# Kernel tuning notes

Measured on AMD Instinct MI355X. Metric: run time of the kernel, lower is better.

Reference implementation:

```python
import jax, jax.numpy as jnp
import numpy as np

B, IN, H = 4096, 1024, 1024

def setup_inputs() -> dict:
    key = jax.random.key(0)
    ks = jax.random.split(key, 8)
    s = 1.0 / np.sqrt(IN + H)  # ~torch Linear init scale
    return {
        "x": jax.random.normal(ks[0], (B, IN), jnp.float32),
        "h_prev": jax.random.normal(ks[1], (B, H), jnp.float32),
        "c_prev": jax.random.normal(ks[2], (B, H), jnp.float32),
        "Wf": jax.random.normal(ks[3], (IN + H, H), jnp.float32) * s,
        "bf": jnp.zeros((H,), jnp.float32),
        "Wi": jax.random.normal(ks[4], (IN + H, H), jnp.float32) * s,
        "bi": jnp.zeros((H,), jnp.float32),
        "Wg": jax.random.normal(ks[5], (IN + H, H), jnp.float32) * s,
        "bg": jnp.zeros((H,), jnp.float32),
        "Wo": jax.random.normal(ks[6], (IN + H, H), jnp.float32) * s,
        "bo": jnp.zeros((H,), jnp.float32),
    }

def reference(x, h_prev, c_prev, Wf, bf, Wi, bi, Wg, bg, Wo, bo):
    combined = jnp.concatenate([x, h_prev], axis=1)          # [B, IN+H]
    # fuse the 4 gate projections into one GEMM: [B, IN+H] x [IN+H, 4H]
    W = jnp.concatenate([Wf, Wi, Wg, Wo], axis=1)            # [IN+H, 4H]
    b = jnp.concatenate([bf, bi, bg, bo], axis=0)            # [4H]
    gates = combined @ W + b                                  # [B, 4H]
    f_t, i_t, g_t, o_t = jnp.split(gates, 4, axis=1)
    f_t = jax.nn.sigmoid(f_t)
    i_t = jax.nn.sigmoid(i_t)
    g_t = jnp.tanh(g_t)
    o_t = jax.nn.sigmoid(o_t)
    c_next = f_t * c_prev + i_t * g_t
    h_next = o_t * jnp.tanh(c_next)
    return (h_next, c_next)
```

## Files before the change

kernel.cpp:

```cpp
#include <hip/hip_runtime.h>

#define B_DIM 4096
#define H_DIM 1024
#define K_DIM 2048

typedef unsigned short u16;
typedef unsigned int u32;
typedef __attribute__((ext_vector_type(8))) short short8;
typedef __attribute__((ext_vector_type(4))) float f32x4;

typedef const __attribute__((address_space(1))) void* gas_ptr;
typedef __attribute__((address_space(3))) void* las_ptr;

#define WT_ELEMS (4 * H_DIM * K_DIM)
#define AC_ELEMS (B_DIM * K_DIM)
#define WS_NEEDED ((size_t)(WT_ELEMS + AC_ELEMS) * 2)

__device__ __forceinline__ void gl_lds16(const u16* g, u16* l) {
    __builtin_amdgcn_global_load_lds((gas_ptr)g, (las_ptr)l, 16, 0, 0);
}
__device__ __forceinline__ float bf2f(u16 v) {
    return __builtin_bit_cast(float, (u32)((u32)v << 16));
}
__device__ __forceinline__ u16 f2bf(float f) {
    u32 u = __builtin_bit_cast(u32, f);
    return (u16)((u + 0x7fffu + ((u >> 16) & 1u)) >> 16);
}
__device__ __forceinline__ float sigm(float x) { return 1.0f / (1.0f + __expf(-x)); }
__device__ __forceinline__ float tanh_f(float x) { return 1.0f - 2.0f / (__expf(2.0f * x) + 1.0f); }

__global__ __launch_bounds__(256) void prep_all(const float* __restrict__ x, const float* __restrict__ h,
                                                const float* __restrict__ Wf, const float* __restrict__ Wi,
                                                const float* __restrict__ Wg, const float* __restrict__ Wo,
                                                u16* __restrict__ A, u16* __restrict__ Wt) {
    __shared__ u16 tl[64][72];
    const int t = threadIdx.x;
    if (blockIdx.x < 4096) {
        int e = (blockIdx.x * 256 + t) * 8;
        int m = e >> 11, c = e & 2047;
        const float* src = (c < 1024) ? (x + (size_t)m * 1024 + c) : (h + (size_t)m * 1024 + (c - 1024));
        float4 v0 = ((const float4*)src)[0], v1 = ((const float4*)src)[1];
        short8 q;
        q[0] = (short)f2bf(v0.x); q[1] = (short)f2bf(v0.y); q[2] = (short)f2bf(v0.z); q[3] = (short)f2bf(v0.w);
        q[4] = (short)f2bf(v1.x); q[5] = (short)f2bf(v1.y); q[6] = (short)f2bf(v1.z); q[7] = (short)f2bf(v1.w);
        *(short8*)(A + e) = q;
    } else {
        int bid = blockIdx.x - 4096;
        const int k0 = (bid & 31) * 64, n0 = ((bid >> 5) & 15) * 64, g = bid >> 9;
        const float* W = (g == 0) ? Wf : (g == 1) ? Wi : (g == 2) ? Wg : Wo;
        {
            int kl = t >> 2, nc = (t & 3) * 16;
            const float4* src = (const float4*)(W + (size_t)(k0 + kl) * H_DIM + n0 + nc);
            float4 v0 = src[0], v1 = src[1], v2 = src[2], v3 = src[3];
            short8 q0, q1;
            q0[0] = (short)f2bf(v0.x); q0[1] = (short)f2bf(v0.y); q0[2] = (short)f2bf(v0.z); q0[3] = (short)f2bf(v0.w);
            q0[4] = (short)f2bf(v1.x); q0[5] = (short)f2bf(v1.y); q0[6] = (short)f2bf(v1.z); q0[7] = (short)f2bf(v1.w);
            q1[0] = (short)f2bf(v2.x); q1[1] = (short)f2bf(v2.y); q1[2] = (short)f2bf(v2.z); q1[3] = (short)f2bf(v2.w);
            q1[4] = (short)f2bf(v3.x); q1[5] = (short)f2bf(v3.y); q1[6] = (short)f2bf(v3.z); q1[7] = (short)f2bf(v3.w);
            *(short8*)&tl[kl][nc] = q0;
            *(short8*)&tl[kl][nc + 8] = q1;
        }
        __syncthreads();
        {
            int nl = t >> 2, kc = (t & 3) * 16;
            short8 r0, r1;
#pragma unroll
            for (int j = 0; j < 8; ++j) { r0[j] = (short)tl[kc + j][nl]; r1[j] = (short)tl[kc + 8 + j][nl]; }
            u16* dst = Wt + (size_t)g * (H_DIM * K_DIM) + (size_t)(n0 + nl) * K_DIM + k0 + kc;
            *(short8*)dst = r0;
            *(short8*)(dst + 8) = r1;
        }
    }
}

__global__ __launch_bounds__(256) void lstm_gemm(
    const u16* __restrict__ A, const u16* __restrict__ Wt, const float* __restrict__ c_prev,
    const float* __restrict__ bf_, const float* __restrict__ bi_,
    const float* __restrict__ bg_, const float* __restrict__ bo_,
    float* __restrict__ out) {
    __shared__ u16 sA[128 * 64];
    __shared__ u16 sB[4 * 32 * 64];

    const int t = threadIdx.x;
    const int w = t >> 6;
    const int l = t & 63;
    const int quad = l >> 4;
    const int l15 = l & 15;
    const int wr = w >> 1;
    const int wc = w & 1;
    const int m0 = blockIdx.x * 128;
    const int j0 = blockIdx.y * 32;

    f32x4 acc[4][4];
#pragma unroll
    for (int g = 0; g < 4; ++g)
#pragma unroll
        for (int mi = 0; mi < 4; ++mi)
            acc[g][mi] = (f32x4){0.f, 0.f, 0.f, 0.f};

    const u16* pA[4];
    const u16* pB[4];
#pragma unroll
    for (int i = 0; i < 4; ++i) {
        int c = i * 256 + t;
        int m = c >> 3, slot = c & 7;
        pA[i] = A + (size_t)(m0 + m) * K_DIM + (slot ^ (m & 7)) * 8;
    }
#pragma unroll
    for (int i = 0; i < 4; ++i) {
        int c = i * 256 + t;
        int g = c >> 8, r = c & 255;
        int n = r >> 3, slot = r & 7;
        pB[i] = Wt + (size_t)g * (H_DIM * K_DIM) + (size_t)(j0 + n) * K_DIM + (slot ^ (n & 7)) * 8;
    }
    const int v7 = l15 & 7;

    for (int kt = 0; kt < K_DIM / 64; ++kt) {
        __syncthreads();
#pragma unroll
        for (int i = 0; i < 4; ++i) {
            gl_lds16(pA[i], sA + (i * 256 + t) * 8);
            pA[i] += 64;
        }
#pragma unroll
        for (int i = 0; i < 4; ++i) {
            gl_lds16(pB[i], sB + (i * 256 + t) * 8);
            pB[i] += 64;
        }
        __syncthreads();

#pragma unroll
        for (int s = 0; s < 2; ++s) {
            const int sl = ((s * 4 + quad) ^ v7) * 8;
            short8 bfr[4];
#pragma unroll
            for (int g = 0; g < 4; ++g)
                bfr[g] = *(const short8*)(sB + g * 2048 + (wc * 16 + l15) * 64 + sl);
            short8 afr[4];
#pragma unroll
            for (int mi = 0; mi < 4; ++mi)
                afr[mi] = *(const short8*)(sA + (wr * 64 + mi * 16 + l15) * 64 + sl);
#pragma unroll
            for (int g = 0; g < 4; ++g)
#pragma unroll
                for (int mi = 0; mi < 4; ++mi)
                    acc[g][mi] = __builtin_amdgcn_mfma_f32_16x16x32_bf16(afr[mi], bfr[g], acc[g][mi], 0, 0, 0);
        }
    }

    const int col = j0 + wc * 16 + l15;
    const float bF = bf_[col], bI = bi_[col], bG = bg_[col], bO = bo_[col];
#pragma unroll
    for (int mi = 0; mi < 4; ++mi) {
        const int rowbase = m0 + wr * 64 + mi * 16 + quad * 4;
        float cp[4];
#pragma unroll
        for (int rr = 0; rr < 4; ++rr)
            cp[rr] = c_prev[(size_t)(rowbase + rr) * H_DIM + col];
#pragma unroll
        for (int rr = 0; rr < 4; ++rr) {
            float fv = sigm(acc[0][mi][rr] + bF);
            float iv = sigm(acc[1][mi][rr] + bI);
            float gv = tanh_f(acc[2][mi][rr] + bG);
            float ov = sigm(acc[3][mi][rr] + bO);
            float cn = fv * cp[rr] + iv * gv;
            float hn = ov * tanh_f(cn);
            size_t idx = (size_t)(rowbase + rr) * H_DIM + col;
            out[idx] = hn;
            out[(size_t)B_DIM * H_DIM + idx] = cn;
        }
    }
}

__global__ __launch_bounds__(256) void lstm_f32(
    const float* __restrict__ x, const float* __restrict__ h_prev, const float* __restrict__ c_prev,
    const float* __restrict__ Wf, const float* __restrict__ Wi, const float* __restrict__ Wg, const float* __restrict__ Wo,
    const float* __restrict__ bf_, const float* __restrict__ bi_, const float* __restrict__ bg_, const float* __restrict__ bo_,
    float* __restrict__ out) {
    __shared__ u16 smem[16384];
    u16* sA = smem;
    u16* sB = smem + 4096;

    const int t = threadIdx.x;
    const int w = t >> 6;
    const int l = t & 63;
    const int quad = l >> 4;
    const int l15 = l & 15;
    const int wr = w >> 1;
    const int wc = w & 1;
    const int m0 = blockIdx.x * 128;
    const int j0 = blockIdx.y * 32;

    const int arow = t >> 1;
    const int akh = (t & 1) * 16;
    const int r7 = t & 127;
    const int bk = r7 >> 2;
    const int bn8 = (r7 & 3) * 8;
    const int kswz = ((((bk >> 3) ^ (bn8 >> 3)) << 3) | (bk & 7));
    const float* WpA = (t < 128) ? Wf : Wi;
    const float* WpB = (t < 128) ? Wg : Wo;
    const int gA = (t >> 7);
    const int gB = 2 + (t >> 7);

    f32x4 acc[2][4][2];
#pragma unroll
    for (int gi = 0; gi < 2; ++gi)
#pragma unroll
        for (int mi = 0; mi < 4; ++mi)
#pragma unroll
            for (int ni = 0; ni < 2; ++ni)
                acc[gi][mi][ni] = (f32x4){0.f, 0.f, 0.f, 0.f};

    for (int kt = 0; kt < K_DIM / 32; ++kt) {
        const float* srcA = (kt < 32) ? x : h_prev;
        const int koff = (kt & 31) * 32;
        __syncthreads();

        const float4* ap = (const float4*)(srcA + (size_t)(m0 + arow) * H_DIM + koff + akh);
        float4 a0 = ap[0], a1 = ap[1], a2 = ap[2], a3 = ap[3];
        short8 p0, p1;
        p0[0] = (short)f2bf(a0.x); p0[1] = (short)f2bf(a0.y); p0[2] = (short)f2bf(a0.z); p0[3] = (short)f2bf(a0.w);
        p0[4] = (short)f2bf(a1.x); p0[5] = (short)f2bf(a1.y); p0[6] = (short)f2bf(a1.z); p0[7] = (short)f2bf(a1.w);
        p1[0] = (short)f2bf(a2.x); p1[1] = (short)f2bf(a2.y); p1[2] = (short)f2bf(a2.z); p1[3] = (short)f2bf(a2.w);
        p1[4] = (short)f2bf(a3.x); p1[5] = (short)f2bf(a3.y); p1[6] = (short)f2bf(a3.z); p1[7] = (short)f2bf(a3.w);
        *(short8*)(sA + arow * 32 + akh) = p0;
        *(short8*)(sA + arow * 32 + akh + 8) = p1;

        const float* gpA = WpA + (size_t)(kt * 32 + bk) * H_DIM + j0 + bn8;
        const float* gpB = WpB + (size_t)(kt * 32 + bk) * H_DIM + j0 + bn8;
        float4 c0 = *(const float4*)gpA, c1 = *(const float4*)(gpA + 4);
        float4 d0 = *(const float4*)gpB, d1 = *(const float4*)(gpB + 4);
        sB[gA * 1024 + (bn8 + 0) * 32 + kswz] = f2bf(c0.x);
        sB[gA * 1024 + (bn8 + 1) * 32 + kswz] = f2bf(c0.y);
        sB[gA * 1024 + (bn8 + 2) * 32 + kswz] = f2bf(c0.z);
        sB[gA * 1024 + (bn8 + 3) * 32 + kswz] = f2bf(c0.w);
        sB[gA * 1024 + (bn8 + 4) * 32 + kswz] = f2bf(c1.x);
        sB[gA * 1024 + (bn8 + 5) * 32 + kswz] = f2bf(c1.y);
        sB[gA * 1024 + (bn8 + 6) * 32 + kswz] = f2bf(c1.z);
        sB[gA * 1024 + (bn8 + 7) * 32 + kswz] = f2bf(c1.w);
        sB[gB * 1024 + (bn8 + 0) * 32 + kswz] = f2bf(d0.x);
        sB[gB * 1024 + (bn8 + 1) * 32 + kswz] = f2bf(d0.y);
        sB[gB * 1024 + (bn8 + 2) * 32 + kswz] = f2bf(d0.z);
        sB[gB * 1024 + (bn8 + 3) * 32 + kswz] = f2bf(d0.w);
        sB[gB * 1024 + (bn8 + 4) * 32 + kswz] = f2bf(d1.x);
        sB[gB * 1024 + (bn8 + 5) * 32 + kswz] = f2bf(d1.y);
        sB[gB * 1024 + (bn8 + 6) * 32 + kswz] = f2bf(d1.z);
        sB[gB * 1024 + (bn8 + 7) * 32 + kswz] = f2bf(d1.w);
        __syncthreads();

        short8 bfr[2][2];
#pragma unroll
        for (int gi = 0; gi < 2; ++gi) {
            int g = wc * 2 + gi;
#pragma unroll
            for (int ni = 0; ni < 2; ++ni) {
                int n = ni * 16 + l15;
                bfr[gi][ni] = *(const short8*)(sB + g * 1024 + n * 32 + ((quad ^ (n >> 3)) * 8));
            }
        }
#pragma unroll
        for (int mi = 0; mi < 4; ++mi) {
            int m = wr * 64 + mi * 16 + l15;
            short8 afr = *(const short8*)(sA + m * 32 + quad * 8);
#pragma unroll
            for (int gi = 0; gi < 2; ++gi)
#pragma unroll
                for (int ni = 0; ni < 2; ++ni)
                    acc[gi][mi][ni] =
                        __builtin_amdgcn_mfma_f32_16x16x32_bf16(afr, bfr[gi][ni], acc[gi][mi][ni], 0, 0, 0);
        }
    }

    __syncthreads();
#pragma unroll
    for (int gi = 0; gi < 2; ++gi) {
        int g = wc * 2 + gi;
        const float* bp = (g == 0) ? bf_ : (g == 1) ? bi_ : (g == 2) ? bg_ : bo_;
#pragma unroll
        for (int ni = 0; ni < 2; ++ni) {
            int col = ni * 16 + l15;
            float bias = bp[j0 + col];
#pragma unroll
            for (int mi = 0; mi < 4; ++mi)
#pragma unroll
                for (int rr = 0; rr < 4; ++rr) {
                    int row = wr * 64 + mi * 16 + quad * 4 + rr;
                    float v = acc[gi][mi][ni][rr] + bias;
                    v = (g == 2) ? tanh_f(v) : sigm(v);
                    smem[g * 4096 + row * 32 + col] = f2bf(v);
                }
        }
    }
    __syncthreads();

    const int col = t & 31;
    const int rb = t >> 5;
#pragma unroll
    for (int p = 0; p < 16; ++p) {
        int row = p * 8 + rb;
        float fv = bf2f(smem[0 * 4096 + row * 32 + col]);
        float iv = bf2f(smem[1 * 4096 + row * 32 + col]);
        float gv = bf2f(smem[2 * 4096 + row * 32 + col]);
        float ov = bf2f(smem[3 * 4096 + row * 32 + col]);
        size_t oidx = (size_t)(m0 + row) * H_DIM + j0 + col;
        float cp = c_prev[oidx];
        float cn = fv * cp + iv * gv;
        float hn = ov * tanh_f(cn);
        out[oidx] = hn;
        out[(size_t)B_DIM * H_DIM + oidx] = cn;
    }
}

extern "C" void kernel_launch(void* const* d_in, const int* in_sizes, int n_in,
                              void* d_out, int out_size, void* d_ws, size_t ws_size,
                              hipStream_t stream) {
    const float* x   = (const float*)d_in[0];
    const float* hp  = (const float*)d_in[1];
    const float* cp  = (const float*)d_in[2];
    const float* Wf  = (const float*)d_in[3];
    const float* bf_ = (const float*)d_in[4];
    const float* Wi  = (const float*)d_in[5];
    const float* bi_ = (const float*)d_in[6];
    const float* Wg  = (const float*)d_in[7];
    const float* bg_ = (const float*)d_in[8];
    const float* Wo  = (const float*)d_in[9];
    const float* bo_ = (const float*)d_in[10];

    if (ws_size >= WS_NEEDED) {
        u16* Wt = (u16*)d_ws;
        u16* Ac = (u16*)d_ws + WT_ELEMS;
        prep_all<<<dim3(4096 + 2048), dim3(256), 0, stream>>>(x, hp, Wf, Wi, Wg, Wo, Ac, Wt);
        lstm_gemm<<<dim3(B_DIM / 128, H_DIM / 32), dim3(256), 0, stream>>>(
            Ac, Wt, cp, bf_, bi_, bg_, bo_, (float*)d_out);
    } else {
        lstm_f32<<<dim3(B_DIM / 128, H_DIM / 32), dim3(256), 0, stream>>>(
            x, hp, cp, Wf, Wi, Wg, Wo, bf_, bi_, bg_, bo_, (float*)d_out);
    }
}
```

Before: 211.9 us.

## Enlarge GEMM block tile to 256 rows with per-warp 64x128 subtiles

Doubles the M tile per block from 128 to 256 rows and changes the warp layout so each warp computes 64 rows across all 32 columns of all four gates (8 N-subtiles), doubling accumulators per thread. This raises arithmetic intensity per LDS load and halves redundant weight tile loads from global memory. It costs more registers and LDS per block, which reduces occupancy; the grid shrinks to 512 blocks, and launch bounds now request 2 blocks per SM.

```diff
diff --git a/kernel.cpp b/kernel.cpp
--- a/kernel.cpp
+++ b/kernel.cpp
@@ -73,12 +73,12 @@
     }
 }
 
-__global__ __launch_bounds__(256) void lstm_gemm(
+__global__ __launch_bounds__(256, 2) void lstm_gemm(
     const u16* __restrict__ A, const u16* __restrict__ Wt, const float* __restrict__ c_prev,
     const float* __restrict__ bf_, const float* __restrict__ bi_,
     const float* __restrict__ bg_, const float* __restrict__ bo_,
     float* __restrict__ out) {
-    __shared__ u16 sA[128 * 64];
+    __shared__ u16 sA[256 * 64];
     __shared__ u16 sB[4 * 32 * 64];
 
     const int t = threadIdx.x;
@@ -86,22 +86,21 @@
     const int l = t & 63;
     const int quad = l >> 4;
     const int l15 = l & 15;
-    const int wr = w >> 1;
-    const int wc = w & 1;
-    const int m0 = blockIdx.x * 128;
+    const int v7 = l15 & 7;
+    const int m0 = blockIdx.x * 256;
     const int j0 = blockIdx.y * 32;
 
-    f32x4 acc[4][4];
-#pragma unroll
-    for (int g = 0; g < 4; ++g)
+    f32x4 acc[8][4];
+#pragma unroll
+    for (int nt = 0; nt < 8; ++nt)
 #pragma unroll
         for (int mi = 0; mi < 4; ++mi)
-            acc[g][mi] = (f32x4){0.f, 0.f, 0.f, 0.f};
-
-    const u16* pA[4];
+            acc[nt][mi] = (f32x4){0.f, 0.f, 0.f, 0.f};
+
+    const u16* pA[8];
     const u16* pB[4];
 #pragma unroll
-    for (int i = 0; i < 4; ++i) {
+    for (int i = 0; i < 8; ++i) {
         int c = i * 256 + t;
         int m = c >> 3, slot = c & 7;
         pA[i] = A + (size_t)(m0 + m) * K_DIM + (slot ^ (m & 7)) * 8;
@@ -113,12 +112,11 @@
         int n = r >> 3, slot = r & 7;
         pB[i] = Wt + (size_t)g * (H_DIM * K_DIM) + (size_t)(j0 + n) * K_DIM + (slot ^ (n & 7)) * 8;
     }
-    const int v7 = l15 & 7;
 
     for (int kt = 0; kt < K_DIM / 64; ++kt) {
         __syncthreads();
 #pragma unroll
-        for (int i = 0; i < 4; ++i) {
+        for (int i = 0; i < 8; ++i) {
             gl_lds16(pA[i], sA + (i * 256 + t) * 8);
             pA[i] += 64;
         }
@@ -132,42 +130,45 @@
 #pragma unroll
         for (int s = 0; s < 2; ++s) {
             const int sl = ((s * 4 + quad) ^ v7) * 8;
-            short8 bfr[4];
-#pragma unroll
-            for (int g = 0; g < 4; ++g)
-                bfr[g] = *(const short8*)(sB + g * 2048 + (wc * 16 + l15) * 64 + sl);
             short8 afr[4];
 #pragma unroll
             for (int mi = 0; mi < 4; ++mi)
-                afr[mi] = *(const short8*)(sA + (wr * 64 + mi * 16 + l15) * 64 + sl);
-#pragma unroll
-            for (int g = 0; g < 4; ++g)
+                afr[mi] = *(const short8*)(sA + (w * 64 + mi * 16 + l15) * 64 + sl);
+            short8 bfr[8];
+#pragma unroll
+            for (int nt = 0; nt < 8; ++nt)
+                bfr[nt] = *(const short8*)(sB + (nt >> 1) * 2048 + ((nt & 1) * 16 + l15) * 64 + sl);
+#pragma unroll
+            for (int nt = 0; nt < 8; ++nt)
 #pragma unroll
                 for (int mi = 0; mi < 4; ++mi)
-                    acc[g][mi] = __builtin_amdgcn_mfma_f32_16x16x32_bf16(afr[mi], bfr[g], acc[g][mi], 0, 0, 0);
-        }
-    }
-
-    const int col = j0 + wc * 16 + l15;
-    const float bF = bf_[col], bI = bi_[col], bG = bg_[col], bO = bo_[col];
-#pragma unroll
-    for (int mi = 0; mi < 4; ++mi) {
-        const int rowbase = m0 + wr * 64 + mi * 16 + quad * 4;
-        float cp[4];
-#pragma unroll
-        for (int rr = 0; rr < 4; ++rr)
-            cp[rr] = c_prev[(size_t)(rowbase + rr) * H_DIM + col];
-#pragma unroll
-        for (int rr = 0; rr < 4; ++rr) {
-            float fv = sigm(acc[0][mi][rr] + bF);
-            float iv = sigm(acc[1][mi][rr] + bI);
-            float gv = tanh_f(acc[2][mi][rr] + bG);
-            float ov = sigm(acc[3][mi][rr] + bO);
-            float cn = fv * cp[rr] + iv * gv;
-            float hn = ov * tanh_f(cn);
-            size_t idx = (size_t)(rowbase + rr) * H_DIM + col;
-            out[idx] = hn;
-            out[(size_t)B_DIM * H_DIM + idx] = cn;
+                    acc[nt][mi] = __builtin_amdgcn_mfma_f32_16x16x32_bf16(afr[mi], bfr[nt], acc[nt][mi], 0, 0, 0);
+        }
+    }
+
+#pragma unroll
+    for (int ni = 0; ni < 2; ++ni) {
+        const int col = j0 + ni * 16 + l15;
+        const float bF = bf_[col], bI = bi_[col], bG = bg_[col], bO = bo_[col];
+#pragma unroll
+        for (int mi = 0; mi < 4; ++mi) {
+            const int rowbase = m0 + w * 64 + mi * 16 + quad * 4;
+            float cp[4];
+#pragma unroll
+            for (int rr = 0; rr < 4; ++rr)
+                cp[rr] = c_prev[(size_t)(rowbase + rr) * H_DIM + col];
+#pragma unroll
+            for (int rr = 0; rr < 4; ++rr) {
+                float fv = sigm(acc[0 + ni][mi][rr] + bF);
+                float iv = sigm(acc[2 + ni][mi][rr] + bI);
+                float gv = tanh_f(acc[4 + ni][mi][rr] + bG);
+                float ov = sigm(acc[6 + ni][mi][rr] + bO);
+                float cn = fv * cp[rr] + iv * gv;
+                float hn = ov * tanh_f(cn);
+                size_t idx = (size_t)(rowbase + rr) * H_DIM + col;
+                out[idx] = hn;
+                out[(size_t)B_DIM * H_DIM + idx] = cn;
+            }
         }
     }
 }
@@ -330,7 +331,7 @@
         u16* Wt = (u16*)d_ws;
         u16* Ac = (u16*)d_ws + WT_ELEMS;
         prep_all<<<dim3(4096 + 2048), dim3(256), 0, stream>>>(x, hp, Wf, Wi, Wg, Wo, Ac, Wt);
-        lstm_gemm<<<dim3(B_DIM / 128, H_DIM / 32), dim3(256), 0, stream>>>(
+        lstm_gemm<<<dim3(B_DIM / 256, H_DIM / 32), dim3(256), 0, stream>>>(
             Ac, Wt, cp, bf_, bi_, bg_, bo_, (float*)d_out);
     } else {
         lstm_f32<<<dim3(B_DIM / 128, H_DIM / 32), dim3(256), 0, stream>>>(
```

Result: faster. 201.0 us (-5.1%).
